# Optimization experiments

Hardware: AMD Instinct MI355X
Metric: run time of the kernel (lower is better)

## Reference

```python
import jax, jax.numpy as jnp
import numpy as np

ROTATION_SHIFT = 15
B, L = 4096, 2048  # batch, code length


def _shift_schedule(r):
    # [0, -1, 1, -2, 2, ..., -r, r] as in the torch loop
    s = [0]
    for x in range(1, r + 1):
        s += [-x, x]
    return jnp.asarray(s, dtype=jnp.int32)


def setup_inputs() -> dict:
    key = jax.random.key(0)
    k1, k2, k3, k4 = jax.random.split(key, 4)
    shape = (2, B, L, 2)
    mk = lambda k: jax.random.randint(k, shape, 0, 2).astype(jnp.bool_)
    return {
        "iris_codes_a": mk(k1),
        "mask_codes_a": mk(k2),
        "iris_codes_b": mk(k3),
        "mask_codes_b": mk(k4),
    }


def reference(iris_codes_a, mask_codes_a, iris_codes_b, mask_codes_b):
    shifts = _shift_schedule(ROTATION_SHIFT)

    def hdist(shift):
        # roll probe codes along the code-length axis (axis=2 of (2,B,L,2))
        ia = jnp.roll(iris_codes_a, shift, axis=2)
        ma = jnp.roll(mask_codes_a, shift, axis=2)
        maskbits = ma & mask_codes_b                      # (2,B,L,2) bool
        irisbits = (ia != iris_codes_b) & maskbits        # masked non-matching bits
        # counts can exceed 2^24, so accumulate in int32 before casting
        num = jnp.sum(irisbits, dtype=jnp.int32).astype(jnp.float32)
        den = jnp.sum(maskbits, dtype=jnp.int32).astype(jnp.float32)
        return num / den

    init = jnp.minimum(jnp.ones((), jnp.float32), hdist(shifts[0]))

    def step(carry, s):
        return jnp.minimum(carry, hdist(s)), None

    match_dist, _ = jax.lax.scan(step, init, shifts[1:])
    return match_dist.reshape(1)  # torch.ones(1) makes the output shape (1,)
```

## Files before the change

### kernel.cpp

```cpp
#include <hip/hip_runtime.h>
#include <stdint.h>

typedef unsigned int u32;

#define NACC   31
#define NSHIFT 15
#define ROWB   4096
#define NBLK   512
#define RPW    4
#define NSH    32

__device__ __forceinline__ void pack16(uint4 v, u32& P0, u32& P1, int t) {
    const u32 q0 = __byte_perm(v.x, v.y, 0x6420);
    const u32 q1 = __byte_perm(v.x, v.y, 0x7531);
    const u32 q2 = __byte_perm(v.z, v.w, 0x6420);
    const u32 q3 = __byte_perm(v.z, v.w, 0x7531);
    const u32 n0 = (q0 * 0x01020408u) >> 24;
    const u32 n1 = (q1 * 0x01020408u) >> 24;
    const u32 n2 = (q2 * 0x01020408u) >> 24;
    const u32 n3 = (q3 * 0x01020408u) >> 24;
    P0 |= (n0 | (n2 << 4)) << (8 * t);
    P1 |= (n1 | (n3 << 4)) << (8 * t);
}

__global__ __launch_bounds__(256, 2) void hd_main(
    const unsigned char* __restrict__ ia, const unsigned char* __restrict__ ma,
    const unsigned char* __restrict__ ib, const unsigned char* __restrict__ mb,
    u32* __restrict__ cnt)
{
    const int tid  = threadIdx.x;
    const int lane = tid & 63;
    const int wv   = tid >> 6;
    const int gw   = blockIdx.x * 4 + wv;

    const int prevL = (lane + 63) & 63;
    const int nextL = (lane + 1) & 63;

    u32 acc[NACC];
#pragma unroll
    for (int j = 0; j < NACC; ++j) acc[j] = 0u;

    const uint4* pa = (const uint4*)(ia + (size_t)gw * RPW * ROWB) + lane * 4;
    const uint4* pm = (const uint4*)(ma + (size_t)gw * RPW * ROWB) + lane * 4;
    const uint4* pb = (const uint4*)(ib + (size_t)gw * RPW * ROWB) + lane * 4;
    const uint4* pn = (const uint4*)(mb + (size_t)gw * RPW * ROWB) + lane * 4;
    const int rstep = ROWB / 16;

    uint4 bA[4], bM[4], bB[4], bN[4];
#pragma unroll
    for (int t = 0; t < 4; ++t) {
        bA[t] = pa[t]; bM[t] = pm[t]; bB[t] = pb[t]; bN[t] = pn[t];
    }

#pragma unroll
    for (int r = 0; r < RPW; ++r) {
        u32 A0 = 0, A1 = 0, M0 = 0, M1 = 0, B0 = 0, B1 = 0, N0 = 0, N1 = 0;
#pragma unroll
        for (int t = 0; t < 4; ++t) {
            pack16(bA[t], A0, A1, t);
            pack16(bM[t], M0, M1, t);
            pack16(bB[t], B0, B1, t);
            pack16(bN[t], N0, N1, t);
        }

        if (r + 1 < RPW) {
            const int o = (r + 1) * rstep;
#pragma unroll
            for (int t = 0; t < 4; ++t) {
                bA[t] = pa[o + t]; bM[t] = pm[o + t];
                bB[t] = pb[o + t]; bN[t] = pn[o + t];
            }
        }

        const u32 pA0 = __shfl(A0, prevL, 64), pA1 = __shfl(A1, prevL, 64);
        const u32 pM0 = __shfl(M0, prevL, 64), pM1 = __shfl(M1, prevL, 64);
        const u32 nA0 = __shfl(A0, nextL, 64), nA1 = __shfl(A1, nextL, 64);
        const u32 nM0 = __shfl(M0, nextL, 64), nM1 = __shfl(M1, nextL, 64);

        {
            const u32 k0 = M0 & N0, k1 = M1 & N1;
            const u32 nm = __popc((A0 ^ B0) & k0) + __popc((A1 ^ B1) & k1);
            const u32 dn = __popc(k0) + __popc(k1);
            acc[15] += nm | (dn << 16);
        }
#pragma unroll
        for (int s = 1; s <= NSHIFT; ++s) {
            {
                const u32 ra0 = (A0 << s) | (pA0 >> (32 - s));
                const u32 ra1 = (A1 << s) | (pA1 >> (32 - s));
                const u32 rm0 = (M0 << s) | (pM0 >> (32 - s));
                const u32 rm1 = (M1 << s) | (pM1 >> (32 - s));
                const u32 k0 = rm0 & N0, k1 = rm1 & N1;
                const u32 nm = __popc((ra0 ^ B0) & k0) + __popc((ra1 ^ B1) & k1);
                const u32 dn = __popc(k0) + __popc(k1);
                acc[15 + s] += nm | (dn << 16);
            }
            {
                const u32 ra0 = (A0 >> s) | (nA0 << (32 - s));
                const u32 ra1 = (A1 >> s) | (nA1 << (32 - s));
                const u32 rm0 = (M0 >> s) | (nM0 << (32 - s));
                const u32 rm1 = (M1 >> s) | (nM1 << (32 - s));
                const u32 k0 = rm0 & N0, k1 = rm1 & N1;
                const u32 nm = __popc((ra0 ^ B0) & k0) + __popc((ra1 ^ B1) & k1);
                const u32 dn = __popc(k0) + __popc(k1);
                acc[15 - s] += nm | (dn << 16);
            }
        }
    }

    __shared__ alignas(16) u32 red[32][132];
#pragma unroll
    for (int j = 0; j < NACC; ++j) acc[j] += __shfl_xor(acc[j], 32, 64);
#pragma unroll
    for (int j = 0; j < NACC; j += 2) {
        const u32 v = (j + 1 < NACC && (lane & 32)) ? acc[j + 1] : acc[j];
        red[j + (lane >> 5)][wv * 32 + (lane & 31)] = v;
    }
    __syncthreads();

    if (tid < 248) {
        const int j = tid >> 3, c = tid & 7;
        const uint4* p = (const uint4*)&red[j][c * 16];
        u32 sn = 0, sd = 0;
#pragma unroll
        for (int i = 0; i < 4; ++i) {
            const uint4 v = p[i];
            sn += (v.x & 0xFFFFu) + (v.y & 0xFFFFu) + (v.z & 0xFFFFu) + (v.w & 0xFFFFu);
            sd += (v.x >> 16) + (v.y >> 16) + (v.z >> 16) + (v.w >> 16);
        }
        sn += __shfl_xor(sn, 1, 64); sd += __shfl_xor(sd, 1, 64);
        sn += __shfl_xor(sn, 2, 64); sd += __shfl_xor(sd, 2, 64);
        sn += __shfl_xor(sn, 4, 64); sd += __shfl_xor(sd, 4, 64);
        if (c == 0) {
            const int sh = blockIdx.x & (NSH - 1);
            atomicAdd(&cnt[j * NSH + sh], sn);
            atomicAdd(&cnt[(31 + j) * NSH + sh], sd);
        }
    }
}

__global__ void hd_finalize(const u32* __restrict__ cnt, float* __restrict__ out)
{
    __shared__ u32 gathered[62];
    const int tid = threadIdx.x;
    if (tid < 248) {
        const int j = tid >> 2, q = tid & 3;
        const uint4* p = (const uint4*)&cnt[j * NSH + q * 8];
        const uint4 v0 = p[0], v1 = p[1];
        u32 s = v0.x + v0.y + v0.z + v0.w + v1.x + v1.y + v1.z + v1.w;
        s += __shfl_xor(s, 1, 64);
        s += __shfl_xor(s, 2, 64);
        if (q == 0) gathered[j] = s;
    }
    __syncthreads();
    if (tid < 64) {
        float f = 1.0f;
        if (tid < NACC) f = (float)gathered[tid] / (float)gathered[31 + tid];
#pragma unroll
        for (int o = 32; o > 0; o >>= 1) f = fminf(f, __shfl_xor(f, o, 64));
        if (tid == 0) out[0] = fminf(f, 1.0f);
    }
}

extern "C" void kernel_launch(void* const* d_in, const int* in_sizes, int n_in,
                              void* d_out, int out_size, void* d_ws, size_t ws_size,
                              hipStream_t stream)
{
    const unsigned char* ia = (const unsigned char*)d_in[0];
    const unsigned char* ma = (const unsigned char*)d_in[1];
    const unsigned char* ib = (const unsigned char*)d_in[2];
    const unsigned char* mb = (const unsigned char*)d_in[3];
    u32* cnt = (u32*)d_ws;

    hipMemsetAsync(d_ws, 0, 62 * NSH * sizeof(u32), stream);
    hd_main<<<dim3(NBLK), dim3(256), 0, stream>>>(ia, ma, ib, mb, cnt);
    hd_finalize<<<dim3(1), dim3(256), 0, stream>>>(cnt, (float*)d_out);
}
```

Measured before the change: 40.25 us.

## Stage input rows through LDS with direct global-to-LDS async loads

Replaces the per-lane uint4 register loads of the four code arrays with __builtin_amdgcn_global_load_lds transfers into a per-wave LDS staging buffer. Each lane then reads its 64 bytes back from LDS before packing, and the next row is prefetched asynchronously after the current row is read. The aim is to make global loads fully coalesced and to free the 16 uint4 prefetch registers. The cost is 64KB of LDS per block, which may cap occupancy, plus an extra LDS round trip and full vmcnt(0) waits that serialise load and compute within a wave.

```diff
diff --git a/kernel.cpp b/kernel.cpp
--- a/kernel.cpp
+++ b/kernel.cpp
@@ -9,6 +9,9 @@
 #define NBLK   512
 #define RPW    4
 #define NSH    32
+
+typedef __attribute__((address_space(3))) unsigned char lds_u8;
+typedef __attribute__((address_space(1))) const unsigned char gbl_u8;
 
 __device__ __forceinline__ void pack16(uint4 v, u32& P0, u32& P1, int t) {
     const u32 q0 = __byte_perm(v.x, v.y, 0x6420);
@@ -33,6 +36,37 @@
     const int wv   = tid >> 6;
     const int gw   = blockIdx.x * 4 + wv;
 
+    __shared__ alignas(16) union {
+        unsigned char stg[4][4][4096];
+        u32 red[32][132];
+    } sh;
+
+#define STAGE_ARR(X, gp) do {                                               \
+        _Pragma("unroll")                                                   \
+        for (int k_ = 0; k_ < 4; ++k_) {                                    \
+            __builtin_amdgcn_global_load_lds(                               \
+                (const gbl_u8*)((gp) + k_ * 1024 + lane * 16),              \
+                (lds_u8*)&sh.stg[wv][X][k_ * 1024], 16, 0, 0);              \
+        }                                                                   \
+    } while (0)
+
+#define STAGE_ROW(rb) do {                                                  \
+        const size_t rb_ = (rb);                                            \
+        STAGE_ARR(0, ia + rb_);                                             \
+        STAGE_ARR(1, ma + rb_);                                             \
+        STAGE_ARR(2, ib + rb_);                                             \
+        STAGE_ARR(3, mb + rb_);                                             \
+    } while (0)
+
+#define LOADPACK(X, P0, P1) do {                                            \
+        P0 = 0u; P1 = 0u;                                                   \
+        _Pragma("unroll")                                                   \
+        for (int j_ = 0; j_ < 4; ++j_) {                                    \
+            const uint4 v_ = *(const uint4*)&sh.stg[wv][X][lane * 64 + j_ * 16]; \
+            pack16(v_, P0, P1, j_);                                         \
+        }                                                                   \
+    } while (0)
+
     const int prevL = (lane + 63) & 63;
     const int nextL = (lane + 1) & 63;
 
@@ -40,37 +74,22 @@
 #pragma unroll
     for (int j = 0; j < NACC; ++j) acc[j] = 0u;
 
-    const uint4* pa = (const uint4*)(ia + (size_t)gw * RPW * ROWB) + lane * 4;
-    const uint4* pm = (const uint4*)(ma + (size_t)gw * RPW * ROWB) + lane * 4;
-    const uint4* pb = (const uint4*)(ib + (size_t)gw * RPW * ROWB) + lane * 4;
-    const uint4* pn = (const uint4*)(mb + (size_t)gw * RPW * ROWB) + lane * 4;
-    const int rstep = ROWB / 16;
-
-    uint4 bA[4], bM[4], bB[4], bN[4];
-#pragma unroll
-    for (int t = 0; t < 4; ++t) {
-        bA[t] = pa[t]; bM[t] = pm[t]; bB[t] = pb[t]; bN[t] = pn[t];
-    }
+    const size_t rowbase0 = (size_t)gw * RPW * ROWB;
+    STAGE_ROW(rowbase0);
 
 #pragma unroll
     for (int r = 0; r < RPW; ++r) {
-        u32 A0 = 0, A1 = 0, M0 = 0, M1 = 0, B0 = 0, B1 = 0, N0 = 0, N1 = 0;
-#pragma unroll
-        for (int t = 0; t < 4; ++t) {
-            pack16(bA[t], A0, A1, t);
-            pack16(bM[t], M0, M1, t);
-            pack16(bB[t], B0, B1, t);
-            pack16(bN[t], N0, N1, t);
-        }
+        asm volatile("s_waitcnt vmcnt(0)" ::: "memory");
+        __builtin_amdgcn_sched_barrier(0);
 
-        if (r + 1 < RPW) {
-            const int o = (r + 1) * rstep;
-#pragma unroll
-            for (int t = 0; t < 4; ++t) {
-                bA[t] = pa[o + t]; bM[t] = pm[o + t];
-                bB[t] = pb[o + t]; bN[t] = pn[o + t];
-            }
-        }
+        u32 A0, A1, M0, M1, B0, B1, N0, N1;
+        LOADPACK(0, A0, A1);
+        LOADPACK(1, M0, M1);
+        LOADPACK(2, B0, B1);
+        LOADPACK(3, N0, N1);
+        __builtin_amdgcn_sched_barrier(0);
+
+        if (r + 1 < RPW) STAGE_ROW(rowbase0 + (size_t)(r + 1) * ROWB);
 
         const u32 pA0 = __shfl(A0, prevL, 64), pA1 = __shfl(A1, prevL, 64);
         const u32 pM0 = __shfl(M0, prevL, 64), pM1 = __shfl(M1, prevL, 64);
@@ -108,19 +127,19 @@
         }
     }
 
-    __shared__ alignas(16) u32 red[32][132];
+    __syncthreads();
 #pragma unroll
     for (int j = 0; j < NACC; ++j) acc[j] += __shfl_xor(acc[j], 32, 64);
 #pragma unroll
     for (int j = 0; j < NACC; j += 2) {
         const u32 v = (j + 1 < NACC && (lane & 32)) ? acc[j + 1] : acc[j];
-        red[j + (lane >> 5)][wv * 32 + (lane & 31)] = v;
+        sh.red[j + (lane >> 5)][wv * 32 + (lane & 31)] = v;
     }
     __syncthreads();
 
     if (tid < 248) {
         const int j = tid >> 3, c = tid & 7;
-        const uint4* p = (const uint4*)&red[j][c * 16];
+        const uint4* p = (const uint4*)&sh.red[j][c * 16];
         u32 sn = 0, sd = 0;
 #pragma unroll
         for (int i = 0; i < 4; ++i) {
@@ -132,9 +151,9 @@
         sn += __shfl_xor(sn, 2, 64); sd += __shfl_xor(sd, 2, 64);
         sn += __shfl_xor(sn, 4, 64); sd += __shfl_xor(sd, 4, 64);
         if (c == 0) {
-            const int sh = blockIdx.x & (NSH - 1);
-            atomicAdd(&cnt[j * NSH + sh], sn);
-            atomicAdd(&cnt[(31 + j) * NSH + sh], sd);
+            const int shd = blockIdx.x & (NSH - 1);
+            atomicAdd(&cnt[j * NSH + shd], sn);
+            atomicAdd(&cnt[(31 + j) * NSH + shd], sd);
         }
     }
 }
```

Result: slower. 41.86 us (+4.0%).

## Coalesce row loads with lane-strided reads and cross-lane bit transpose

Applied to the files above, without the earlier changes.

Each wave now processes one row instead of four. Lanes load 16-byte chunks at stride 64 (t*64+lane) so each load instruction is fully coalesced, rather than each lane reading 64 contiguous bytes. The packed bits are then redistributed across lanes with shuffles and byte permutes so that each lane still holds a contiguous 64-bit span. Grid size grows fourfold and occupancy is raised to 4 blocks per CU. The cost is extra shuffle and permute work per row, more partial-sum atomics, and no in-wave prefetch of the next row.

```diff
diff --git a/kernel.cpp b/kernel.cpp
--- a/kernel.cpp
+++ b/kernel.cpp
@@ -6,11 +6,10 @@
 #define NACC   31
 #define NSHIFT 15
 #define ROWB   4096
-#define NBLK   512
-#define RPW    4
+#define NBLK   2048
 #define NSH    32
 
-__device__ __forceinline__ void pack16(uint4 v, u32& P0, u32& P1, int t) {
+__device__ __forceinline__ u32 chunk16(uint4 v) {
     const u32 q0 = __byte_perm(v.x, v.y, 0x6420);
     const u32 q1 = __byte_perm(v.x, v.y, 0x7531);
     const u32 q2 = __byte_perm(v.z, v.w, 0x6420);
@@ -19,11 +18,27 @@
     const u32 n1 = (q1 * 0x01020408u) >> 24;
     const u32 n2 = (q2 * 0x01020408u) >> 24;
     const u32 n3 = (q3 * 0x01020408u) >> 24;
-    P0 |= (n0 | (n2 << 4)) << (8 * t);
-    P1 |= (n1 | (n3 << 4)) << (8 * t);
+    return (n0 | (n2 << 4)) | ((n1 | (n3 << 4)) << 8);
 }
 
-__global__ __launch_bounds__(256, 2) void hd_main(
+__device__ __forceinline__ void packarr(const uint4 s[4], u32& PL0, u32& PL1) {
+    const u32 c0 = chunk16(s[0]), c1 = chunk16(s[1]);
+    const u32 c2 = chunk16(s[2]), c3 = chunk16(s[3]);
+    const u32 lo01 = __byte_perm(c0, c1, 0x5410);
+    const u32 lo23 = __byte_perm(c2, c3, 0x5410);
+    PL0 = __byte_perm(lo01, lo23, 0x6420);
+    PL1 = __byte_perm(lo01, lo23, 0x7531);
+}
+
+__device__ __forceinline__ void xpose(u32 PL, int s0, u32 selE, u32& W) {
+    const u32 g0 = __shfl(PL, s0, 64),     g1 = __shfl(PL, s0 + 1, 64);
+    const u32 g2 = __shfl(PL, s0 + 2, 64), g3 = __shfl(PL, s0 + 3, 64);
+    const u32 p01 = __byte_perm(g0, g1, selE);
+    const u32 p23 = __byte_perm(g2, g3, selE);
+    W = __byte_perm(p01, p23, 0x5410);
+}
+
+__global__ __launch_bounds__(256, 4) void hd_main(
     const unsigned char* __restrict__ ia, const unsigned char* __restrict__ ma,
     const unsigned char* __restrict__ ib, const unsigned char* __restrict__ mb,
     u32* __restrict__ cnt)
@@ -31,80 +46,75 @@
     const int tid  = threadIdx.x;
     const int lane = tid & 63;
     const int wv   = tid >> 6;
-    const int gw   = blockIdx.x * 4 + wv;
+    const int row  = blockIdx.x * 4 + wv;
 
-    const int prevL = (lane + 63) & 63;
-    const int nextL = (lane + 1) & 63;
+    const size_t rb = (size_t)row * ROWB;
+    const uint4* pa = (const uint4*)(ia + rb);
+    const uint4* pm = (const uint4*)(ma + rb);
+    const uint4* pb = (const uint4*)(ib + rb);
+    const uint4* pn = (const uint4*)(mb + rb);
+
+    uint4 sA[4], sM[4], sB[4], sN[4];
+#pragma unroll
+    for (int t = 0; t < 4; ++t) sA[t] = pa[t * 64 + lane];
+#pragma unroll
+    for (int t = 0; t < 4; ++t) sM[t] = pm[t * 64 + lane];
+#pragma unroll
+    for (int t = 0; t < 4; ++t) sB[t] = pb[t * 64 + lane];
+#pragma unroll
+    for (int t = 0; t < 4; ++t) sN[t] = pn[t * 64 + lane];
+
+    const int s0   = (lane << 2) & 63;
+    const u32 e    = (u32)(lane >> 4);
+    const u32 selE = e | ((e + 4u) << 4);
+
+    u32 A0, A1, M0, M1, B0, B1, N0, N1;
+    {
+        u32 L0, L1;
+        packarr(sA, L0, L1); xpose(L0, s0, selE, A0); xpose(L1, s0, selE, A1);
+        packarr(sM, L0, L1); xpose(L0, s0, selE, M0); xpose(L1, s0, selE, M1);
+        packarr(sB, L0, L1); xpose(L0, s0, selE, B0); xpose(L1, s0, selE, B1);
+        packarr(sN, L0, L1); xpose(L0, s0, selE, N0); xpose(L1, s0, selE, N1);
+    }
 
     u32 acc[NACC];
 #pragma unroll
     for (int j = 0; j < NACC; ++j) acc[j] = 0u;
 
-    const uint4* pa = (const uint4*)(ia + (size_t)gw * RPW * ROWB) + lane * 4;
-    const uint4* pm = (const uint4*)(ma + (size_t)gw * RPW * ROWB) + lane * 4;
-    const uint4* pb = (const uint4*)(ib + (size_t)gw * RPW * ROWB) + lane * 4;
-    const uint4* pn = (const uint4*)(mb + (size_t)gw * RPW * ROWB) + lane * 4;
-    const int rstep = ROWB / 16;
+    const int prevL = (lane + 63) & 63;
+    const int nextL = (lane + 1) & 63;
+    const u32 pA0 = __shfl(A0, prevL, 64), pA1 = __shfl(A1, prevL, 64);
+    const u32 pM0 = __shfl(M0, prevL, 64), pM1 = __shfl(M1, prevL, 64);
+    const u32 nA0 = __shfl(A0, nextL, 64), nA1 = __shfl(A1, nextL, 64);
+    const u32 nM0 = __shfl(M0, nextL, 64), nM1 = __shfl(M1, nextL, 64);
 
-    uint4 bA[4], bM[4], bB[4], bN[4];
+    {
+        const u32 k0 = M0 & N0, k1 = M1 & N1;
+        const u32 nm = __popc((A0 ^ B0) & k0) + __popc((A1 ^ B1) & k1);
+        const u32 dn = __popc(k0) + __popc(k1);
+        acc[15] += nm | (dn << 16);
+    }
 #pragma unroll
-    for (int t = 0; t < 4; ++t) {
-        bA[t] = pa[t]; bM[t] = pm[t]; bB[t] = pb[t]; bN[t] = pn[t];
-    }
-
-#pragma unroll
-    for (int r = 0; r < RPW; ++r) {
-        u32 A0 = 0, A1 = 0, M0 = 0, M1 = 0, B0 = 0, B1 = 0, N0 = 0, N1 = 0;
-#pragma unroll
-        for (int t = 0; t < 4; ++t) {
-            pack16(bA[t], A0, A1, t);
-            pack16(bM[t], M0, M1, t);
-            pack16(bB[t], B0, B1, t);
-            pack16(bN[t], N0, N1, t);
+    for (int s = 1; s <= NSHIFT; ++s) {
+        {
+            const u32 ra0 = (A0 << s) | (pA0 >> (32 - s));
+            const u32 ra1 = (A1 << s) | (pA1 >> (32 - s));
+            const u32 rm0 = (M0 << s) | (pM0 >> (32 - s));
+            const u32 rm1 = (M1 << s) | (pM1 >> (32 - s));
+            const u32 k0 = rm0 & N0, k1 = rm1 & N1;
+            const u32 nm = __popc((ra0 ^ B0) & k0) + __popc((ra1 ^ B1) & k1);
+            const u32 dn = __popc(k0) + __popc(k1);
+            acc[15 + s] += nm | (dn << 16);
         }
-
-        if (r + 1 < RPW) {
-            const int o = (r + 1) * rstep;
-#pragma unroll
-            for (int t = 0; t < 4; ++t) {
-                bA[t] = pa[o + t]; bM[t] = pm[o + t];
-                bB[t] = pb[o + t]; bN[t] = pn[o + t];
-            }
-        }
-
-        const u32 pA0 = __shfl(A0, prevL, 64), pA1 = __shfl(A1, prevL, 64);
-        const u32 pM0 = __shfl(M0, prevL, 64), pM1 = __shfl(M1, prevL, 64);
-        const u32 nA0 = __shfl(A0, nextL, 64), nA1 = __shfl(A1, nextL, 64);
-        const u32 nM0 = __shfl(M0, nextL, 64), nM1 = __shfl(M1, nextL, 64);
-
         {
-            const u32 k0 = M0 & N0, k1 = M1 & N1;
-            const u32 nm = __popc((A0 ^ B0) & k0) + __popc((A1 ^ B1) & k1);
+            const u32 ra0 = (A0 >> s) | (nA0 << (32 - s));
+            const u32 ra1 = (A1 >> s) | (nA1 << (32 - s));
+            const u32 rm0 = (M0 >> s) | (nM0 << (32 - s));
+            const u32 rm1 = (M1 >> s) | (nM1 << (32 - s));
+            const u32 k0 = rm0 & N0, k1 = rm1 & N1;
+            const u32 nm = __popc((ra0 ^ B0) & k0) + __popc((ra1 ^ B1) & k1);
             const u32 dn = __popc(k0) + __popc(k1);
-            acc[15] += nm | (dn << 16);
-        }
-#pragma unroll
-        for (int s = 1; s <= NSHIFT; ++s) {
-            {
-                const u32 ra0 = (A0 << s) | (pA0 >> (32 - s));
-                const u32 ra1 = (A1 << s) | (pA1 >> (32 - s));
-                const u32 rm0 = (M0 << s) | (pM0 >> (32 - s));
-                const u32 rm1 = (M1 << s) | (pM1 >> (32 - s));
-                const u32 k0 = rm0 & N0, k1 = rm1 & N1;
-                const u32 nm = __popc((ra0 ^ B0) & k0) + __popc((ra1 ^ B1) & k1);
-                const u32 dn = __popc(k0) + __popc(k1);
-                acc[15 + s] += nm | (dn << 16);
-            }
-            {
-                const u32 ra0 = (A0 >> s) | (nA0 << (32 - s));
-                const u32 ra1 = (A1 >> s) | (nA1 << (32 - s));
-                const u32 rm0 = (M0 >> s) | (nM0 << (32 - s));
-                const u32 rm1 = (M1 >> s) | (nM1 << (32 - s));
-                const u32 k0 = rm0 & N0, k1 = rm1 & N1;
-                const u32 nm = __popc((ra0 ^ B0) & k0) + __popc((ra1 ^ B1) & k1);
-                const u32 dn = __popc(k0) + __popc(k1);
-                acc[15 - s] += nm | (dn << 16);
-            }
+            acc[15 - s] += nm | (dn << 16);
         }
     }
 
```

Measured after the change: 53.37 us. 32.6% more time.
